# Optimization experiments

Hardware: AMD Instinct MI355X
Metric: run time of the kernel (lower is better)

## Reference

```python
import jax, jax.numpy as jnp
import numpy as np

B, LATENT, LOCAL, HIDDEN, H, W = 512, 256, 256, 512, 16, 16


def setup_inputs() -> dict:
    key = jax.random.key(0)
    ks = jax.random.split(key, 7)
    anchor = jax.random.normal(ks[0], (B, LATENT), dtype=jnp.float32)
    positive = jax.random.normal(ks[1], (B, LOCAL, H, W), dtype=jnp.float32)
    # MLP params (Linear: y = x @ W + b), scaled like Kaiming-uniform-ish init
    W1 = jax.random.normal(ks[2], (LATENT, HIDDEN), dtype=jnp.float32) / np.sqrt(LATENT)
    b1 = jnp.zeros((HIDDEN,), dtype=jnp.float32)
    W2 = jax.random.normal(ks[3], (HIDDEN, LATENT), dtype=jnp.float32) / np.sqrt(HIDDEN)
    b2 = jnp.zeros((LATENT,), dtype=jnp.float32)
    # self.W: Linear(latent -> local, bias=False)
    Wc = jax.random.normal(ks[4], (LATENT, LOCAL), dtype=jnp.float32) / np.sqrt(LATENT)
    return {"anchor": anchor, "positive": positive, "W1": W1, "b1": b1,
            "W2": W2, "b2": b2, "Wc": Wc}


def reference(anchor, positive, W1, b1, W2, b2, Wc):
    # residual MLP on anchor: anchor + MLP(anchor)
    a = anchor + (jax.nn.relu(anchor @ W1 + b1) @ W2 + b2)  # [b, latent]
    pred = a @ Wc                                            # [b, local]
    b, c, h, w = positive.shape
    pos = positive.reshape(b, c, h * w)                      # [b, c, hw]
    # fused batched matmul over all h*w locations:
    # logits[k, i, j] = sum_c pred[i, c] * positive[j, c, k]
    logits = jnp.einsum('ic,jck->kij', pred, pos)            # [hw, b, b]
    # row-wise max subtraction (over the contrast dim, dim=1 in torch)
    logits = logits - jnp.max(logits, axis=2, keepdims=True)
    return logits  # stacked version of the torch list of h*w [b, b] matrices
```

## Files before the change

### kernel.cpp

```cpp
#include <hip/hip_runtime.h>
#include <hip/hip_bf16.h>

typedef unsigned short u16;
typedef unsigned int u32;
typedef __attribute__((ext_vector_type(8))) short short8;
typedef __attribute__((ext_vector_type(4))) float f32x4;

#define B_   512
#define C_   256
#define HID_ 512
#define HW_  256

__device__ __forceinline__ u16 f2b(float f) {
    union { float f; u32 i; } v; v.f = f;
    u32 x = v.i;
    u32 r = (x + 0x7fffu + ((x >> 16) & 1u)) >> 16;
    return (u16)r;
}
__device__ __forceinline__ float b2f(u16 u) {
    union { u32 i; float f; } v; v.i = ((u32)u) << 16; return v.f;
}

__device__ __forceinline__ void dma16(const u16* g, u16* l) {
    __builtin_amdgcn_global_load_lds(
        (const __attribute__((address_space(1))) u32*)g,
        (__attribute__((address_space(3))) u32*)l, 16, 0, 0);
}

__global__ __launch_bounds__(256) void k_mlp(
        const float* __restrict__ anchor, const float* __restrict__ W1,
        const float* __restrict__ b1, const float* __restrict__ W2,
        const float* __restrict__ b2, const float* __restrict__ Wc,
        u16* __restrict__ pred)
{
    const int row0 = blockIdx.x * 4, t = threadIdx.x;
    __shared__ float a_sh[4][C_];
    __shared__ float h_sh[4][HID_];
    __shared__ float a2_sh[4][C_];

    #pragma unroll
    for (int r = 0; r < 4; ++r) a_sh[r][t] = anchor[(size_t)(row0 + r) * C_ + t];
    __syncthreads();

    float h0[4], h1[4];
    {
        float2 bb = *(const float2*)&b1[2 * t];
        #pragma unroll
        for (int r = 0; r < 4; ++r) { h0[r] = bb.x; h1[r] = bb.y; }
    }
    for (int l = 0; l < C_; ++l) {
        float2 w = *(const float2*)&W1[(size_t)l * HID_ + 2 * t];
        #pragma unroll
        for (int r = 0; r < 4; ++r) {
            float a = a_sh[r][l];
            h0[r] += a * w.x;
            h1[r] += a * w.y;
        }
    }
    #pragma unroll
    for (int r = 0; r < 4; ++r) {
        h_sh[r][2 * t]     = fmaxf(h0[r], 0.f);
        h_sh[r][2 * t + 1] = fmaxf(h1[r], 0.f);
    }
    __syncthreads();

    float a2[4];
    {
        float bv = b2[t];
        #pragma unroll
        for (int r = 0; r < 4; ++r) a2[r] = a_sh[r][t] + bv;
    }
    for (int h = 0; h < HID_; ++h) {
        float w = W2[(size_t)h * C_ + t];
        #pragma unroll
        for (int r = 0; r < 4; ++r) a2[r] += h_sh[r][h] * w;
    }
    #pragma unroll
    for (int r = 0; r < 4; ++r) a2_sh[r][t] = a2[r];
    __syncthreads();

    float p[4] = {0.f, 0.f, 0.f, 0.f};
    for (int d = 0; d < C_; ++d) {
        float w = Wc[(size_t)d * C_ + t];
        #pragma unroll
        for (int r = 0; r < 4; ++r) p[r] += a2_sh[r][d] * w;
    }
    #pragma unroll
    for (int r = 0; r < 4; ++r) pred[(size_t)(row0 + r) * C_ + t] = f2b(p[r]);
}

__global__ __launch_bounds__(256) void k_transpose(
        const float* __restrict__ positive, u16* __restrict__ P)
{
    const int bx = blockIdx.x;
    const int j  = bx >> 2;
    const int k0 = (bx & 3) * 64;
    const int t  = threadIdx.x;

    __shared__ float Tf[64][68];

    const float* pj = positive + (size_t)j * (C_ * HW_);

    for (int p = 0; p < 4; ++p) {
        const int c0 = p * 64;
        {
            const int kk = t & 15, cr = t >> 4;
            #pragma unroll
            for (int s = 0; s < 4; ++s) {
                const int cl = s * 16 + cr;
                float4 v = *(const float4*)&pj[(size_t)(c0 + cl) * HW_ + k0 + kk * 4];
                *(float4*)&Tf[cl][kk * 4] = v;
            }
        }
        __syncthreads();
        {
            const int kr = t >> 2, cq = t & 3;
            u32 wpk[8];
            #pragma unroll
            for (int y = 0; y < 16; y += 2) {
                u16 lo = f2b(Tf[cq * 16 + y][kr]);
                u16 hi = f2b(Tf[cq * 16 + y + 1][kr]);
                wpk[y >> 1] = (u32)lo | ((u32)hi << 16);
            }
            u16* dst = P + ((size_t)(k0 + kr) * B_ + j) * C_ + c0 + cq * 16;
            ((uint4*)dst)[0] = make_uint4(wpk[0], wpk[1], wpk[2], wpk[3]);
            ((uint4*)dst)[1] = make_uint4(wpk[4], wpk[5], wpk[6], wpk[7]);
        }
        __syncthreads();
    }
}

__global__ __launch_bounds__(512, 2) void k_gemm_fused(
        const u16* __restrict__ P, const u16* __restrict__ pred,
        float* __restrict__ out)
{
    const int bx = blockIdx.x;
    const int k  = bx >> 2;
    const int i0 = (bx & 3) * 128;

    __shared__ u16 Bsm[B_ * 32];
    __shared__ u16 Asm[128 * 32];
    __shared__ float maxw[128][4];
    __shared__ float maxv[128];

    const int tid  = threadIdx.x;
    const int lane = tid & 63, w = tid >> 6;
    const int q = lane >> 4, m = lane & 15;
    const int wi = w >> 2, wj = w & 3;

    const u16* Pk = P + (size_t)k * (B_ * C_);

    f32x4 acc[4][8];
    #pragma unroll
    for (int a = 0; a < 4; ++a)
        #pragma unroll
        for (int b = 0; b < 8; ++b) acc[a][b] = f32x4{0.f, 0.f, 0.f, 0.f};

    for (int ch = 0; ch < 8; ++ch) {
        const int c0 = ch * 32;
        __syncthreads();
        #pragma unroll
        for (int r = 0; r < 4; ++r) {
            const int jb  = w * 64 + r * 16 + (lane >> 2);
            const int oct = lane & 3;
            dma16(Pk + (size_t)jb * C_ + c0 + oct * 8,
                  Bsm + (size_t)(w * 256 + r * 64) * 8);
        }
        {
            const int ia  = w * 16 + (lane >> 2);
            const int oct = lane & 3;
            dma16(pred + (size_t)(i0 + ia) * C_ + c0 + oct * 8,
                  Asm + (size_t)(w * 64) * 8);
        }
        __syncthreads();

        union { uint4 u; short8 v; } af[4], bf[8];
        #pragma unroll
        for (int mt = 0; mt < 4; ++mt)
            af[mt].u = *(const uint4*)&Asm[((wi * 64 + mt * 16 + m) * 4 + q) * 8];
        #pragma unroll
        for (int nt = 0; nt < 8; ++nt)
            bf[nt].u = *(const uint4*)&Bsm[((wj * 128 + nt * 16 + m) * 4 + q) * 8];
        #pragma unroll
        for (int mt = 0; mt < 4; ++mt)
            #pragma unroll
            for (int nt = 0; nt < 8; ++nt)
                acc[mt][nt] = __builtin_amdgcn_mfma_f32_16x16x32_bf16(
                    af[mt].v, bf[nt].v, acc[mt][nt], 0, 0, 0);
    }

    float pm[4][4];
    #pragma unroll
    for (int mt = 0; mt < 4; ++mt)
        #pragma unroll
        for (int r = 0; r < 4; ++r) {
            float v = acc[mt][0][r];
            #pragma unroll
            for (int nt = 1; nt < 8; ++nt) v = fmaxf(v, acc[mt][nt][r]);
            pm[mt][r] = v;
        }
    #pragma unroll
    for (int d = 1; d < 16; d <<= 1) {
        #pragma unroll
        for (int mt = 0; mt < 4; ++mt)
            #pragma unroll
            for (int r = 0; r < 4; ++r)
                pm[mt][r] = fmaxf(pm[mt][r], __shfl_xor(pm[mt][r], d, 64));
    }
    __syncthreads();
    if (m == 0) {
        #pragma unroll
        for (int mt = 0; mt < 4; ++mt)
            #pragma unroll
            for (int r = 0; r < 4; ++r)
                maxw[wi * 64 + mt * 16 + q * 4 + r][wj] = pm[mt][r];
    }
    __syncthreads();
    if (tid < 128)
        maxv[tid] = fmaxf(fmaxf(maxw[tid][0], maxw[tid][1]),
                          fmaxf(maxw[tid][2], maxw[tid][3]));
    __syncthreads();

    #pragma unroll
    for (int mt = 0; mt < 4; ++mt) {
        #pragma unroll
        for (int r = 0; r < 4; ++r) {
            const int i_ = i0 + wi * 64 + mt * 16 + q * 4 + r;
            const float mv = maxv[wi * 64 + mt * 16 + q * 4 + r];
            float* orow = out + ((size_t)k * B_ + i_) * B_ + wj * 128;
            #pragma unroll
            for (int nt = 0; nt < 8; ++nt)
                orow[nt * 16 + m] = acc[mt][nt][r] - mv;
        }
    }
}

extern "C" void kernel_launch(void* const* d_in, const int* in_sizes, int n_in,
                              void* d_out, int out_size, void* d_ws, size_t ws_size,
                              hipStream_t stream)
{
    const float* anchor   = (const float*)d_in[0];
    const float* positive = (const float*)d_in[1];
    const float* W1 = (const float*)d_in[2];
    const float* b1 = (const float*)d_in[3];
    const float* W2 = (const float*)d_in[4];
    const float* b2 = (const float*)d_in[5];
    const float* Wc = (const float*)d_in[6];
    float* out = (float*)d_out;

    u16* pred = (u16*)d_ws;
    u16* P    = (u16*)((char*)d_ws + (size_t)B_ * C_ * 2);

    k_mlp<<<B_ / 4, 256, 0, stream>>>(anchor, W1, b1, W2, b2, Wc, pred);
    k_transpose<<<B_ * 4, 256, 0, stream>>>(positive, P);
    k_gemm_fused<<<HW_ * 4, 512, 0, stream>>>(P, pred, out);
}
```

Baseline: 507.0 us.

## Double-buffer GEMM B tiles, preload full A tile, widen blocks and remap k

The fused GEMM kernel moves to 1024-thread blocks with 16 waves. It loads the whole 128x256 pred tile into swizzled LDS once, then streams the P tiles through a double buffer, with explicit vmcnt waits and barriers so the next DMA overlaps the MFMAs. The block-to-k mapping is permuted, likely to spread k across XCDs or cache. The MLP kernel is also split across 512 threads with partial-sum reductions. The risks are heavier LDS use per block, more barriers and fewer accumulators per wave.

```diff
diff --git a/kernel.cpp b/kernel.cpp
--- a/kernel.cpp
+++ b/kernel.cpp
@@ -27,7 +27,7 @@
         (__attribute__((address_space(3))) u32*)l, 16, 0, 0);
 }
 
-__global__ __launch_bounds__(256) void k_mlp(
+__global__ __launch_bounds__(512) void k_mlp(
         const float* __restrict__ anchor, const float* __restrict__ W1,
         const float* __restrict__ b1, const float* __restrict__ W2,
         const float* __restrict__ b2, const float* __restrict__ Wc,
@@ -36,57 +36,70 @@
     const int row0 = blockIdx.x * 4, t = threadIdx.x;
     __shared__ float a_sh[4][C_];
     __shared__ float h_sh[4][HID_];
+    __shared__ float part[2][4][C_];
     __shared__ float a2_sh[4][C_];
 
-    #pragma unroll
-    for (int r = 0; r < 4; ++r) a_sh[r][t] = anchor[(size_t)(row0 + r) * C_ + t];
-    __syncthreads();
-
-    float h0[4], h1[4];
-    {
-        float2 bb = *(const float2*)&b1[2 * t];
-        #pragma unroll
-        for (int r = 0; r < 4; ++r) { h0[r] = bb.x; h1[r] = bb.y; }
-    }
-    for (int l = 0; l < C_; ++l) {
-        float2 w = *(const float2*)&W1[(size_t)l * HID_ + 2 * t];
-        #pragma unroll
-        for (int r = 0; r < 4; ++r) {
-            float a = a_sh[r][l];
-            h0[r] += a * w.x;
-            h1[r] += a * w.y;
-        }
-    }
-    #pragma unroll
-    for (int r = 0; r < 4; ++r) {
-        h_sh[r][2 * t]     = fmaxf(h0[r], 0.f);
-        h_sh[r][2 * t + 1] = fmaxf(h1[r], 0.f);
-    }
-    __syncthreads();
-
-    float a2[4];
-    {
-        float bv = b2[t];
-        #pragma unroll
-        for (int r = 0; r < 4; ++r) a2[r] = a_sh[r][t] + bv;
-    }
-    for (int h = 0; h < HID_; ++h) {
-        float w = W2[(size_t)h * C_ + t];
-        #pragma unroll
-        for (int r = 0; r < 4; ++r) a2[r] += h_sh[r][h] * w;
-    }
-    #pragma unroll
-    for (int r = 0; r < 4; ++r) a2_sh[r][t] = a2[r];
-    __syncthreads();
-
-    float p[4] = {0.f, 0.f, 0.f, 0.f};
-    for (int d = 0; d < C_; ++d) {
-        float w = Wc[(size_t)d * C_ + t];
-        #pragma unroll
-        for (int r = 0; r < 4; ++r) p[r] += a2_sh[r][d] * w;
-    }
-    #pragma unroll
-    for (int r = 0; r < 4; ++r) pred[(size_t)(row0 + r) * C_ + t] = f2b(p[r]);
+    {
+        const int r = t >> 8, c = t & 255;
+        a_sh[r][c]     = anchor[(size_t)(row0 + r) * C_ + c];
+        a_sh[r + 2][c] = anchor[(size_t)(row0 + r + 2) * C_ + c];
+    }
+    __syncthreads();
+
+    {
+        float h0 = b1[t], h1 = h0, h2 = h0, h3 = h0;
+        #pragma unroll 4
+        for (int l = 0; l < C_; ++l) {
+            float wv = W1[(size_t)l * HID_ + t];
+            h0 += a_sh[0][l] * wv; h1 += a_sh[1][l] * wv;
+            h2 += a_sh[2][l] * wv; h3 += a_sh[3][l] * wv;
+        }
+        h_sh[0][t] = fmaxf(h0, 0.f); h_sh[1][t] = fmaxf(h1, 0.f);
+        h_sh[2][t] = fmaxf(h2, 0.f); h_sh[3][t] = fmaxf(h3, 0.f);
+    }
+    __syncthreads();
+
+    {
+        const int c = t & 255, hh = t >> 8;
+        float s0 = 0.f, s1 = 0.f, s2 = 0.f, s3 = 0.f;
+        #pragma unroll 4
+        for (int x = 0; x < 256; ++x) {
+            const int h = hh * 256 + x;
+            float wv = W2[(size_t)h * C_ + c];
+            s0 += h_sh[0][h] * wv; s1 += h_sh[1][h] * wv;
+            s2 += h_sh[2][h] * wv; s3 += h_sh[3][h] * wv;
+        }
+        part[hh][0][c] = s0; part[hh][1][c] = s1;
+        part[hh][2][c] = s2; part[hh][3][c] = s3;
+    }
+    __syncthreads();
+    if (t < 256) {
+        const float bv = b2[t];
+        #pragma unroll
+        for (int r = 0; r < 4; ++r)
+            a2_sh[r][t] = a_sh[r][t] + bv + part[0][r][t] + part[1][r][t];
+    }
+    __syncthreads();
+
+    {
+        const int c = t & 255, dh = t >> 8;
+        float s0 = 0.f, s1 = 0.f, s2 = 0.f, s3 = 0.f;
+        #pragma unroll 4
+        for (int x = 0; x < 128; ++x) {
+            const int d = dh * 128 + x;
+            float wv = Wc[(size_t)d * C_ + c];
+            s0 += a2_sh[0][d] * wv; s1 += a2_sh[1][d] * wv;
+            s2 += a2_sh[2][d] * wv; s3 += a2_sh[3][d] * wv;
+        }
+        part[dh][0][c] = s0; part[dh][1][c] = s1;
+        part[dh][2][c] = s2; part[dh][3][c] = s3;
+    }
+    __syncthreads();
+    if (t < 256) {
+        #pragma unroll
+        for (int r = 0; r < 4; ++r)
+            pred[(size_t)(row0 + r) * C_ + t] = f2b(part[0][r][t] + part[1][r][t]);
+    }
 }
 
 __global__ __launch_bounds__(256) void k_transpose(
@@ -130,63 +143,82 @@
     }
 }
 
-__global__ __launch_bounds__(512, 2) void k_gemm_fused(
+__global__ __launch_bounds__(1024, 4) void k_gemm_fused(
         const u16* __restrict__ P, const u16* __restrict__ pred,
         float* __restrict__ out)
 {
-    const int bx = blockIdx.x;
-    const int k  = bx >> 2;
-    const int i0 = (bx & 3) * 128;
-
-    __shared__ u16 Bsm[B_ * 32];
-    __shared__ u16 Asm[128 * 32];
-    __shared__ float maxw[128][4];
+    const int b  = blockIdx.x;
+    const int k  = (b & 7) * 32 + (b >> 5);
+    const int i0 = ((b >> 3) & 3) * 128;
+
+    __shared__ u16 Asm[128 * 256];
+    __shared__ u16 Bsm[2][1024 * 8];
+    __shared__ float maxw[128][8];
     __shared__ float maxv[128];
 
     const int tid  = threadIdx.x;
     const int lane = tid & 63, w = tid >> 6;
     const int q = lane >> 4, m = lane & 15;
-    const int wi = w >> 2, wj = w & 3;
+    const int wi = w >> 3, wj = w & 7;
 
     const u16* Pk = P + (size_t)k * (B_ * C_);
 
-    f32x4 acc[4][8];
+    {
+        const int usrc = (tid & 31) ^ ((tid >> 5) & 7);
+        const u16* asrc = pred + (size_t)(i0 + (tid >> 5)) * C_ + usrc * 8;
+        #pragma unroll
+        for (int r = 0; r < 4; ++r)
+            dma16(asrc + (size_t)r * 32 * C_,
+                  Asm + (size_t)(r * 1024 + w * 64) * 8);
+    }
+    const int jr_base = (tid >> 7) * 64 + ((tid >> 2) & 31);
+    const int osw     = (tid & 3) ^ ((tid >> 3) & 3);
+    const u16* bsrc   = Pk + (size_t)jr_base * C_ + osw * 8;
+
+    dma16(bsrc, Bsm[0] + (size_t)w * 64 * 8);
+
+    const int bq   = q ^ ((m >> 1) & 3);
+    const int brd0 = ((wj * 32 + m) * 4 + bq) * 8;
+    const int ard0 = (wi * 64 + m) * 256;
+
+    union U { uint4 u; short8 v; };
+    U af[4];
+    f32x4 acc[4][4];
     #pragma unroll
     for (int a = 0; a < 4; ++a)
         #pragma unroll
-        for (int b = 0; b < 8; ++b) acc[a][b] = f32x4{0.f, 0.f, 0.f, 0.f};
-
-    for (int ch = 0; ch < 8; ++ch) {
-        const int c0 = ch * 32;
-        __syncthreads();
-        #pragma unroll
-        for (int r = 0; r < 4; ++r) {
-            const int jb  = w * 64 + r * 16 + (lane >> 2);
-            const int oct = lane & 3;
-            dma16(Pk + (size_t)jb * C_ + c0 + oct * 8,
-                  Bsm + (size_t)(w * 256 + r * 64) * 8);
-        }
-        {
-            const int ia  = w * 16 + (lane >> 2);
-            const int oct = lane & 3;
-            dma16(pred + (size_t)(i0 + ia) * C_ + c0 + oct * 8,
-                  Asm + (size_t)(w * 64) * 8);
-        }
-        __syncthreads();
-
-        union { uint4 u; short8 v; } af[4], bf[8];
-        #pragma unroll
-        for (int mt = 0; mt < 4; ++mt)
-            af[mt].u = *(const uint4*)&Asm[((wi * 64 + mt * 16 + m) * 4 + q) * 8];
-        #pragma unroll
-        for (int nt = 0; nt < 8; ++nt)
-            bf[nt].u = *(const uint4*)&Bsm[((wj * 128 + nt * 16 + m) * 4 + q) * 8];
-        #pragma unroll
-        for (int mt = 0; mt < 4; ++mt)
-            #pragma unroll
-            for (int nt = 0; nt < 8; ++nt)
-                acc[mt][nt] = __builtin_amdgcn_mfma_f32_16x16x32_bf16(
-                    af[mt].v, bf[nt].v, acc[mt][nt], 0, 0, 0);
+        for (int bb = 0; bb < 4; ++bb) acc[a][bb] = f32x4{0.f, 0.f, 0.f, 0.f};
+
+    #pragma unroll
+    for (int g = 0; g < 16; ++g) {
+        if (g < 15) {
+            const int gn = g + 1, chn = gn >> 1, hn = gn & 1;
+            dma16(bsrc + (size_t)hn * 32 * C_ + chn * 32,
+                  Bsm[gn & 1] + (size_t)w * 64 * 8);
+            asm volatile("s_waitcnt vmcnt(1)" ::: "memory");
+        } else {
+            asm volatile("s_waitcnt vmcnt(0)" ::: "memory");
+        }
+        __builtin_amdgcn_s_barrier();
+        asm volatile("" ::: "memory");
+
+        const int ch = g >> 1, h = g & 1;
+        if (h == 0) {
+            const int x = ((ch * 4 + q) ^ (m & 7)) * 8;
+            #pragma unroll
+            for (int mt = 0; mt < 4; ++mt)
+                af[mt].u = *(const uint4*)&Asm[ard0 + mt * 4096 + x];
+        }
+        #pragma unroll
+        for (int n = 0; n < 2; ++n) {
+            U bf; bf.u = *(const uint4*)&Bsm[g & 1][brd0 + n * 512];
+            #pragma unroll
+            for (int mt = 0; mt < 4; ++mt)
+                acc[mt][2 * h + n] = __builtin_amdgcn_mfma_f32_16x16x32_bf16(
+                    af[mt].v, bf.v, acc[mt][2 * h + n], 0, 0, 0);
+        }
+        asm volatile("" ::: "memory");
+        __builtin_amdgcn_s_barrier();
     }
 
     float pm[4][4];
@@ -196,7 +228,7 @@
         for (int r = 0; r < 4; ++r) {
             float v = acc[mt][0][r];
             #pragma unroll
-            for (int nt = 1; nt < 8; ++nt) v = fmaxf(v, acc[mt][nt][r]);
+            for (int nt = 1; nt < 4; ++nt) v = fmaxf(v, acc[mt][nt][r]);
             pm[mt][r] = v;
         }
     #pragma unroll
@@ -216,20 +248,23 @@
                 maxw[wi * 64 + mt * 16 + q * 4 + r][wj] = pm[mt][r];
     }
     __syncthreads();
-    if (tid < 128)
-        maxv[tid] = fmaxf(fmaxf(maxw[tid][0], maxw[tid][1]),
-                          fmaxf(maxw[tid][2], maxw[tid][3]));
+    if (tid < 128) {
+        float v = maxw[tid][0];
+        #pragma unroll
+        for (int x = 1; x < 8; ++x) v = fmaxf(v, maxw[tid][x]);
+        maxv[tid] = v;
+    }
     __syncthreads();
 
     #pragma unroll
     for (int mt = 0; mt < 4; ++mt) {
         #pragma unroll
         for (int r = 0; r < 4; ++r) {
-            const int i_ = i0 + wi * 64 + mt * 16 + q * 4 + r;
-            const float mv = maxv[wi * 64 + mt * 16 + q * 4 + r];
-            float* orow = out + ((size_t)k * B_ + i_) * B_ + wj * 128;
-            #pragma unroll
-            for (int nt = 0; nt < 8; ++nt)
+            const int il = wi * 64 + mt * 16 + q * 4 + r;
+            const float mv = maxv[il];
+            float* orow = out + ((size_t)k * B_ + i0 + il) * B_ + wj * 64;
+            #pragma unroll
+            for (int nt = 0; nt < 4; ++nt)
                 orow[nt * 16 + m] = acc[mt][nt][r] - mv;
         }
     }
@@ -251,7 +286,7 @@
     u16* pred = (u16*)d_ws;
     u16* P    = (u16*)((char*)d_ws + (size_t)B_ * C_ * 2);
 
-    k_mlp<<<B_ / 4, 256, 0, stream>>>(anchor, W1, b1, W2, b2, Wc, pred);
+    k_mlp<<<B_ / 4, 512, 0, stream>>>(anchor, W1, b1, W2, b2, Wc, pred);
     k_transpose<<<B_ * 4, 256, 0, stream>>>(positive, P);
-    k_gemm_fused<<<HW_ * 4, 512, 0, stream>>>(P, pred, out);
-}
+    k_gemm_fused<<<1024, 1024, 0, stream>>>(P, pred, out);
+}
```

Measured after the change: 514.2 us. No clear change (+1.4%).
